# Performance work log

Measured on AMD Instinct MI355X. Metric: run time of the kernel, lower is better.

Reference implementation:

```python
import jax, jax.numpy as jnp
import numpy as np

NODE_DIM, HIDDEN_DIM, OUT_DIM = 64, 128, 64
N_NODES, N_EDGES = 50000, 800000
SLOPE = 0.05


def leaky(x):
    return jnp.where(x >= 0, x, SLOPE * x)


def setup_inputs() -> dict:
    key = jax.random.key(0)
    ks = jax.random.split(key, 8)
    x = jax.random.normal(ks[0], (N_NODES, NODE_DIM), dtype=jnp.float32)
    edge_index = jax.random.randint(ks[1], (2, N_EDGES), 0, N_NODES, dtype=jnp.int64)
    s0 = 1.0 / np.sqrt(NODE_DIM)
    s1 = 1.0 / np.sqrt(HIDDEN_DIM)
    W0 = jax.random.uniform(ks[2], (NODE_DIM, HIDDEN_DIM), jnp.float32, -s0, s0)
    b0 = jax.random.uniform(ks[3], (HIDDEN_DIM,), jnp.float32, -s0, s0)
    W1 = jax.random.uniform(ks[4], (HIDDEN_DIM, HIDDEN_DIM), jnp.float32, -s1, s1)
    b1 = jax.random.uniform(ks[5], (HIDDEN_DIM,), jnp.float32, -s1, s1)
    W2 = jax.random.uniform(ks[6], (HIDDEN_DIM, OUT_DIM), jnp.float32, -s1, s1)
    b2 = jax.random.uniform(ks[7], (OUT_DIM,), jnp.float32, -s1, s1)
    return {"x": x, "edge_index": edge_index, "W0": W0, "b0": b0,
            "W1": W1, "b1": b1, "W2": W2, "b2": b2}


def reference(x, edge_index, W0, b0, W1, b1, W2, b2):
    # gather-sum: [E, node_dim]
    e = x[edge_index[0]] + x[edge_index[1]]
    h = leaky(e @ W0 + b0)          # [E, hidden]
    h = leaky(h @ W1 + b1)          # [E, hidden]
    out = leaky(h @ W2 + b2)        # [E, out]
    return out
```

## Files before the change

### kernel.cpp

```cpp
#include <hip/hip_runtime.h>

typedef _Float16 half8  __attribute__((ext_vector_type(8)));
typedef float    floatx4 __attribute__((ext_vector_type(4)));

#define N_NODES 50000
#define N_EDGES 800000
#define SLOPE 0.05f

#define WS_Z   0ull
#define WS_W1  (WS_Z  + (size_t)N_NODES * 128 * 2)
#define WS_W2  (WS_W1 + 128 * 128 * 2)
#define WS_B0  (WS_W2 + 64 * 128 * 2)
#define WS_B1  (WS_B0 + 128 * 4)
#define WS_B2  (WS_B1 + 128 * 4)

#define W0_STRIDE 72
#define H_STRIDE 136
#define HC_STRIDE 40

__device__ __forceinline__ float leaky(float t) { return t >= 0.f ? t : SLOPE * t; }

__global__ void wprep_kernel(const float* __restrict__ W1, const float* __restrict__ W2,
                             const float* __restrict__ b0, const float* __restrict__ b1,
                             const float* __restrict__ b2, unsigned char* __restrict__ ws) {
    _Float16* wt1 = (_Float16*)(ws + WS_W1);
    _Float16* wt2 = (_Float16*)(ws + WS_W2);
    float* B0 = (float*)(ws + WS_B0);
    float* B1 = (float*)(ws + WS_B1);
    float* B2 = (float*)(ws + WS_B2);
    int t = blockIdx.x * 1024 + threadIdx.x;
    if (t < 16384) {
        int k = t >> 7, n = t & 127;
        wt1[n * 128 + k] = (_Float16)W1[k * 128 + n];
    } else if (t < 24576) {
        int i = t - 16384;
        int k = i >> 6, n = i & 63;
        wt2[n * 128 + k] = (_Float16)W2[k * 64 + n];
    } else if (t < 24576 + 320) {
        int i = t - 24576;
        if (i < 128) B0[i] = b0[i];
        else if (i < 256) B1[i - 128] = b1[i - 128];
        else B2[i - 256] = b2[i - 256];
    }
}

__global__ __launch_bounds__(512, 4) void z_kernel(const float* __restrict__ x,
                                                   const float* __restrict__ W0,
                                                   unsigned char* __restrict__ ws) {
    __shared__ __align__(16) _Float16 w0t[128 * W0_STRIDE];
    __shared__ __align__(16) _Float16 hbuf[8][16 * H_STRIDE];
    _Float16* __restrict__ z = (_Float16*)(ws + WS_Z);

    {
        int t = threadIdx.x;
        int n = t >> 2, k0 = (t & 3) * 16;
        half8 t0, t1;
        #pragma unroll
        for (int j = 0; j < 8; ++j) t0[j] = (_Float16)W0[(k0 + j) * 128 + n];
        #pragma unroll
        for (int j = 0; j < 8; ++j) t1[j] = (_Float16)W0[(k0 + 8 + j) * 128 + n];
        *(half8*)&w0t[n * W0_STRIDE + k0] = t0;
        *(half8*)&w0t[n * W0_STRIDE + k0 + 8] = t1;
    }
    __syncthreads();

    const int wave = threadIdx.x >> 6, lane = threadIdx.x & 63;
    const int cl = lane & 15, q = lane >> 4;
    const int rowbase = blockIdx.x * 128 + wave * 16;
    int row = rowbase + cl; if (row > N_NODES - 1) row = N_NODES - 1;

    half8 a[2];
    #pragma unroll
    for (int ks = 0; ks < 2; ++ks) {
        const floatx4* px = (const floatx4*)(x + (size_t)row * 64 + ks * 32 + q * 8);
        floatx4 u0 = px[0], u1 = px[1];
        #pragma unroll
        for (int j = 0; j < 4; ++j) { a[ks][j] = (_Float16)u0[j]; a[ks][4 + j] = (_Float16)u1[j]; }
    }

    _Float16* hs = &hbuf[wave][0];
    #pragma unroll
    for (int n = 0; n < 8; ++n) {
        floatx4 c = {0.f, 0.f, 0.f, 0.f};
        #pragma unroll
        for (int ks = 0; ks < 2; ++ks) {
            half8 b = *(const half8*)&w0t[(n * 16 + cl) * W0_STRIDE + ks * 32 + q * 8];
            c = __builtin_amdgcn_mfma_f32_16x16x32_f16(a[ks], b, c, 0, 0, 0);
        }
        #pragma unroll
        for (int r = 0; r < 4; ++r)
            hs[(q * 4 + r) * H_STRIDE + n * 16 + cl] = (_Float16)c[r];
    }

    int rl = lane >> 2, ch = lane & 3;
    int grow = rowbase + rl;
    if (grow < N_NODES) {
        #pragma unroll
        for (int i = 0; i < 4; ++i)
            *(half8*)(z + (size_t)grow * 128 + i * 32 + ch * 8) =
                *(const half8*)&hs[rl * H_STRIDE + i * 32 + ch * 8];
    }
}

__global__ __launch_bounds__(512, 4) void edge_kernel(const int* __restrict__ ei,
                                                      const unsigned char* __restrict__ ws,
                                                      float* __restrict__ out) {
    __shared__ __align__(16) _Float16 w1s[128 * H_STRIDE];
    __shared__ __align__(16) _Float16 w2s[64 * H_STRIDE];
    __shared__ __align__(16) _Float16 hc[8][16 * HC_STRIDE];
    __shared__ float b0s[128], b1s[128], b2s[64];

    const _Float16* __restrict__ z    = (const _Float16*)(ws + WS_Z);
    const _Float16* __restrict__ wt1g = (const _Float16*)(ws + WS_W1);
    const _Float16* __restrict__ wt2g = (const _Float16*)(ws + WS_W2);

    {
        int t = threadIdx.x;
        #pragma unroll
        for (int it = 0; it < 4; ++it) {
            int c = t + it * 512;
            int row = c >> 4, cc = c & 15;
            *(half8*)&w1s[row * H_STRIDE + cc * 8] = *(const half8*)&wt1g[row * 128 + cc * 8];
        }
        #pragma unroll
        for (int it = 0; it < 2; ++it) {
            int c = t + it * 512;
            int row = c >> 4, cc = c & 15;
            *(half8*)&w2s[row * H_STRIDE + cc * 8] = *(const half8*)&wt2g[row * 128 + cc * 8];
        }
        if (t < 128) {
            b0s[t] = *(const float*)(ws + WS_B0 + t * 4);
            b1s[t] = *(const float*)(ws + WS_B1 + t * 4);
        } else if (t < 192) {
            b2s[t - 128] = *(const float*)(ws + WS_B2 + (size_t)(t - 128) * 4);
        }
    }
    __syncthreads();

    const int wave = threadIdx.x >> 6, lane = threadIdx.x & 63;
    const int cl = lane & 15, q = lane >> 4;
    const int rowbase = blockIdx.x * 128 + wave * 16;

    const int r = rowbase + cl;
    const int s = ei[r];
    const int d = ei[N_EDGES + r];
    const _Float16* zs = z + (size_t)s * 128;
    const _Float16* zd = z + (size_t)d * 128;

    half8 a1[4];
    #pragma unroll
    for (int ks = 0; ks < 4; ++ks) {
        half8 u = *(const half8*)(zs + ks * 32 + q * 8);
        half8 v = *(const half8*)(zd + ks * 32 + q * 8);
        floatx4 bA = *(const floatx4*)&b0s[ks * 32 + q * 8];
        floatx4 bB = *(const floatx4*)&b0s[ks * 32 + q * 8 + 4];
        #pragma unroll
        for (int j = 0; j < 4; ++j) {
            float t0 = (float)u[j]     + (float)v[j]     + bA[j];
            float t1 = (float)u[4 + j] + (float)v[4 + j] + bB[j];
            a1[ks][j]     = (_Float16)leaky(t0);
            a1[ks][4 + j] = (_Float16)leaky(t1);
        }
    }

    _Float16* hw = &hc[wave][0];
    floatx4 acc2[4];
    #pragma unroll
    for (int n2 = 0; n2 < 4; ++n2) acc2[n2] = (floatx4){0.f, 0.f, 0.f, 0.f};

    #pragma unroll
    for (int ks = 0; ks < 4; ++ks) {
        #pragma unroll
        for (int nn = 0; nn < 2; ++nn) {
            const int n = ks * 2 + nn;
            floatx4 c = {0.f, 0.f, 0.f, 0.f};
            #pragma unroll
            for (int kk = 0; kk < 4; ++kk) {
                half8 b = *(const half8*)&w1s[(n * 16 + cl) * H_STRIDE + kk * 32 + q * 8];
                c = __builtin_amdgcn_mfma_f32_16x16x32_f16(a1[kk], b, c, 0, 0, 0);
            }
            const float bb = b1s[n * 16 + cl];
            #pragma unroll
            for (int rr = 0; rr < 4; ++rr)
                hw[(q * 4 + rr) * HC_STRIDE + nn * 16 + cl] = (_Float16)leaky(c[rr] + bb);
        }
        half8 a2 = *(const half8*)&hw[cl * HC_STRIDE + q * 8];
        #pragma unroll
        for (int n2 = 0; n2 < 4; ++n2) {
            half8 b = *(const half8*)&w2s[(n2 * 16 + cl) * H_STRIDE + ks * 32 + q * 8];
            acc2[n2] = __builtin_amdgcn_mfma_f32_16x16x32_f16(a2, b, acc2[n2], 0, 0, 0);
        }
    }

    #pragma unroll
    for (int n2 = 0; n2 < 4; ++n2) {
        const float bb = b2s[n2 * 16 + cl];
        #pragma unroll
        for (int rr = 0; rr < 4; ++rr)
            out[(size_t)(rowbase + q * 4 + rr) * 64 + n2 * 16 + cl] = leaky(acc2[n2][rr] + bb);
    }
}

extern "C" void kernel_launch(void* const* d_in, const int* in_sizes, int n_in,
                              void* d_out, int out_size, void* d_ws, size_t ws_size,
                              hipStream_t stream) {
    const float* x  = (const float*)d_in[0];
    const int*   ei = (const int*)d_in[1];
    const float* W0 = (const float*)d_in[2];
    const float* b0 = (const float*)d_in[3];
    const float* W1 = (const float*)d_in[4];
    const float* b1 = (const float*)d_in[5];
    const float* W2 = (const float*)d_in[6];
    const float* b2 = (const float*)d_in[7];
    float* out = (float*)d_out;
    unsigned char* ws = (unsigned char*)d_ws;

    wprep_kernel<<<25, 1024, 0, stream>>>(W1, W2, b0, b1, b2, ws);
    z_kernel<<<(N_NODES + 127) / 128, 512, 0, stream>>>(x, W0, ws);
    edge_kernel<<<N_EDGES / 128, 512, 0, stream>>>(ei, ws, out);
}
```

Baseline: 295.3 us.

## Make edge kernel persistent with two M-tiles per wave and index prefetch

```diff
diff --git a/kernel.cpp b/kernel.cpp
--- a/kernel.cpp
+++ b/kernel.cpp
@@ -6,6 +6,8 @@
 #define N_NODES 50000
 #define N_EDGES 800000
 #define SLOPE 0.05f
+#define GRID 512
+#define NT 3125
 
 #define WS_Z   0ull
 #define WS_W1  (WS_Z  + (size_t)N_NODES * 128 * 2)
@@ -13,6 +15,7 @@
 #define WS_B0  (WS_W2 + 64 * 128 * 2)
 #define WS_B1  (WS_B0 + 128 * 4)
 #define WS_B2  (WS_B1 + 128 * 4)
+#define WS_W0T (WS_B2 + 64 * 4)
 
 #define W0_STRIDE 72
 #define H_STRIDE 136
@@ -20,11 +23,13 @@
 
 __device__ __forceinline__ float leaky(float t) { return t >= 0.f ? t : SLOPE * t; }
 
-__global__ void wprep_kernel(const float* __restrict__ W1, const float* __restrict__ W2,
-                             const float* __restrict__ b0, const float* __restrict__ b1,
-                             const float* __restrict__ b2, unsigned char* __restrict__ ws) {
+__global__ void wprep_kernel(const float* __restrict__ W0, const float* __restrict__ W1,
+                             const float* __restrict__ W2, const float* __restrict__ b0,
+                             const float* __restrict__ b1, const float* __restrict__ b2,
+                             unsigned char* __restrict__ ws) {
     _Float16* wt1 = (_Float16*)(ws + WS_W1);
     _Float16* wt2 = (_Float16*)(ws + WS_W2);
+    _Float16* w0t = (_Float16*)(ws + WS_W0T);
     float* B0 = (float*)(ws + WS_B0);
     float* B1 = (float*)(ws + WS_B1);
     float* B2 = (float*)(ws + WS_B2);
@@ -36,8 +41,12 @@
         int i = t - 16384;
         int k = i >> 6, n = i & 63;
         wt2[n * 128 + k] = (_Float16)W2[k * 64 + n];
-    } else if (t < 24576 + 320) {
+    } else if (t < 32768) {
         int i = t - 24576;
+        int n = i >> 6, k = i & 63;
+        w0t[n * 64 + k] = (_Float16)W0[k * 128 + n];
+    } else if (t < 32768 + 320) {
+        int i = t - 32768;
         if (i < 128) B0[i] = b0[i];
         else if (i < 256) B1[i - 128] = b1[i - 128];
         else B2[i - 256] = b2[i - 256];
@@ -45,22 +54,20 @@
 }
 
 __global__ __launch_bounds__(512, 4) void z_kernel(const float* __restrict__ x,
-                                                   const float* __restrict__ W0,
                                                    unsigned char* __restrict__ ws) {
-    __shared__ __align__(16) _Float16 w0t[128 * W0_STRIDE];
+    __shared__ __align__(16) _Float16 w0s[128 * W0_STRIDE];
     __shared__ __align__(16) _Float16 hbuf[8][16 * H_STRIDE];
     _Float16* __restrict__ z = (_Float16*)(ws + WS_Z);
+    const _Float16* __restrict__ w0t = (const _Float16*)(ws + WS_W0T);
 
     {
         int t = threadIdx.x;
-        int n = t >> 2, k0 = (t & 3) * 16;
-        half8 t0, t1;
-        #pragma unroll
-        for (int j = 0; j < 8; ++j) t0[j] = (_Float16)W0[(k0 + j) * 128 + n];
-        #pragma unroll
-        for (int j = 0; j < 8; ++j) t1[j] = (_Float16)W0[(k0 + 8 + j) * 128 + n];
-        *(half8*)&w0t[n * W0_STRIDE + k0] = t0;
-        *(half8*)&w0t[n * W0_STRIDE + k0 + 8] = t1;
+        #pragma unroll
+        for (int it = 0; it < 2; ++it) {
+            int c = t + it * 512;
+            int row = c >> 3, cc = c & 7;
+            *(half8*)&w0s[row * W0_STRIDE + cc * 8] = *(const half8*)&w0t[row * 64 + cc * 8];
+        }
     }
     __syncthreads();
 
@@ -84,7 +91,7 @@
         floatx4 c = {0.f, 0.f, 0.f, 0.f};
         #pragma unroll
         for (int ks = 0; ks < 2; ++ks) {
-            half8 b = *(const half8*)&w0t[(n * 16 + cl) * W0_STRIDE + ks * 32 + q * 8];
+            half8 b = *(const half8*)&w0s[(n * 16 + cl) * W0_STRIDE + ks * 32 + q * 8];
             c = __builtin_amdgcn_mfma_f32_16x16x32_f16(a[ks], b, c, 0, 0, 0);
         }
         #pragma unroll
@@ -139,65 +146,107 @@
 
     const int wave = threadIdx.x >> 6, lane = threadIdx.x & 63;
     const int cl = lane & 15, q = lane >> 4;
-    const int rowbase = blockIdx.x * 128 + wave * 16;
-
-    const int r = rowbase + cl;
-    const int s = ei[r];
-    const int d = ei[N_EDGES + r];
-    const _Float16* zs = z + (size_t)s * 128;
-    const _Float16* zd = z + (size_t)d * 128;
-
-    half8 a1[4];
-    #pragma unroll
-    for (int ks = 0; ks < 4; ++ks) {
-        half8 u = *(const half8*)(zs + ks * 32 + q * 8);
-        half8 v = *(const half8*)(zd + ks * 32 + q * 8);
-        floatx4 bA = *(const floatx4*)&b0s[ks * 32 + q * 8];
-        floatx4 bB = *(const floatx4*)&b0s[ks * 32 + q * 8 + 4];
-        #pragma unroll
-        for (int j = 0; j < 4; ++j) {
-            float t0 = (float)u[j]     + (float)v[j]     + bA[j];
-            float t1 = (float)u[4 + j] + (float)v[4 + j] + bB[j];
-            a1[ks][j]     = (_Float16)leaky(t0);
-            a1[ks][4 + j] = (_Float16)leaky(t1);
-        }
-    }
-
     _Float16* hw = &hc[wave][0];
-    floatx4 acc2[4];
-    #pragma unroll
-    for (int n2 = 0; n2 < 4; ++n2) acc2[n2] = (floatx4){0.f, 0.f, 0.f, 0.f};
-
-    #pragma unroll
-    for (int ks = 0; ks < 4; ++ks) {
-        #pragma unroll
-        for (int nn = 0; nn < 2; ++nn) {
-            const int n = ks * 2 + nn;
-            floatx4 c = {0.f, 0.f, 0.f, 0.f};
-            #pragma unroll
-            for (int kk = 0; kk < 4; ++kk) {
-                half8 b = *(const half8*)&w1s[(n * 16 + cl) * H_STRIDE + kk * 32 + q * 8];
-                c = __builtin_amdgcn_mfma_f32_16x16x32_f16(a1[kk], b, c, 0, 0, 0);
-            }
-            const float bb = b1s[n * 16 + cl];
-            #pragma unroll
-            for (int rr = 0; rr < 4; ++rr)
-                hw[(q * 4 + rr) * HC_STRIDE + nn * 16 + cl] = (_Float16)leaky(c[rr] + bb);
-        }
-        half8 a2 = *(const half8*)&hw[cl * HC_STRIDE + q * 8];
+
+    int tile = blockIdx.x;
+    int s0, d0, s1, d1;
+    {
+        int r = tile * 256 + wave * 32 + cl;
+        s0 = ei[r];           d0 = ei[N_EDGES + r];
+        s1 = ei[r + 16];      d1 = ei[N_EDGES + r + 16];
+    }
+
+    while (tile < NT) {
+        const int next = tile + GRID;
+        int ns0 = s0, nd0 = d0, ns1 = s1, nd1 = d1;
+        if (next < NT) {
+            int r = next * 256 + wave * 32 + cl;
+            ns0 = ei[r];      nd0 = ei[N_EDGES + r];
+            ns1 = ei[r + 16]; nd1 = ei[N_EDGES + r + 16];
+        }
+
+        const int eb = tile * 256 + wave * 32;
+
+        const _Float16* zs0 = z + (size_t)s0 * 128;
+        const _Float16* zd0 = z + (size_t)d0 * 128;
+        const _Float16* zs1 = z + (size_t)s1 * 128;
+        const _Float16* zd1 = z + (size_t)d1 * 128;
+
+        half8 a1lo[4], a1hi[4];
+        #pragma unroll
+        for (int ks = 0; ks < 4; ++ks) {
+            half8 u = *(const half8*)(zs0 + ks * 32 + q * 8);
+            half8 v = *(const half8*)(zd0 + ks * 32 + q * 8);
+            half8 u2 = *(const half8*)(zs1 + ks * 32 + q * 8);
+            half8 v2 = *(const half8*)(zd1 + ks * 32 + q * 8);
+            floatx4 bA = *(const floatx4*)&b0s[ks * 32 + q * 8];
+            floatx4 bB = *(const floatx4*)&b0s[ks * 32 + q * 8 + 4];
+            #pragma unroll
+            for (int j = 0; j < 4; ++j) {
+                a1lo[ks][j]     = (_Float16)leaky((float)u[j]      + (float)v[j]      + bA[j]);
+                a1lo[ks][4 + j] = (_Float16)leaky((float)u[4 + j]  + (float)v[4 + j]  + bB[j]);
+                a1hi[ks][j]     = (_Float16)leaky((float)u2[j]     + (float)v2[j]     + bA[j]);
+                a1hi[ks][4 + j] = (_Float16)leaky((float)u2[4 + j] + (float)v2[4 + j] + bB[j]);
+            }
+        }
+
+        floatx4 acc2lo[4], acc2hi[4];
         #pragma unroll
         for (int n2 = 0; n2 < 4; ++n2) {
-            half8 b = *(const half8*)&w2s[(n2 * 16 + cl) * H_STRIDE + ks * 32 + q * 8];
-            acc2[n2] = __builtin_amdgcn_mfma_f32_16x16x32_f16(a2, b, acc2[n2], 0, 0, 0);
-        }
-    }
-
-    #pragma unroll
-    for (int n2 = 0; n2 < 4; ++n2) {
-        const float bb = b2s[n2 * 16 + cl];
-        #pragma unroll
-        for (int rr = 0; rr < 4; ++rr)
-            out[(size_t)(rowbase + q * 4 + rr) * 64 + n2 * 16 + cl] = leaky(acc2[n2][rr] + bb);
+            acc2lo[n2] = (floatx4){0.f, 0.f, 0.f, 0.f};
+            acc2hi[n2] = (floatx4){0.f, 0.f, 0.f, 0.f};
+        }
+
+        #pragma unroll
+        for (int ks = 0; ks < 4; ++ks) {
+            floatx4 kc[2];
+            #pragma unroll
+            for (int nn = 0; nn < 2; ++nn) {
+                const int n = ks * 2 + nn;
+                floatx4 c0 = {0.f, 0.f, 0.f, 0.f};
+                floatx4 c1 = {0.f, 0.f, 0.f, 0.f};
+                #pragma unroll
+                for (int kk = 0; kk < 4; ++kk) {
+                    half8 b = *(const half8*)&w1s[(n * 16 + cl) * H_STRIDE + kk * 32 + q * 8];
+                    c0 = __builtin_amdgcn_mfma_f32_16x16x32_f16(a1lo[kk], b, c0, 0, 0, 0);
+                    c1 = __builtin_amdgcn_mfma_f32_16x16x32_f16(a1hi[kk], b, c1, 0, 0, 0);
+                }
+                const float bb = b1s[n * 16 + cl];
+                #pragma unroll
+                for (int rr = 0; rr < 4; ++rr)
+                    hw[(q * 4 + rr) * HC_STRIDE + nn * 16 + cl] = (_Float16)leaky(c0[rr] + bb);
+                kc[nn] = c1;
+            }
+            half8 a2lo = *(const half8*)&hw[cl * HC_STRIDE + q * 8];
+            #pragma unroll
+            for (int nn = 0; nn < 2; ++nn) {
+                const float bb = b1s[(ks * 2 + nn) * 16 + cl];
+                #pragma unroll
+                for (int rr = 0; rr < 4; ++rr)
+                    hw[(q * 4 + rr) * HC_STRIDE + nn * 16 + cl] = (_Float16)leaky(kc[nn][rr] + bb);
+            }
+            half8 a2hi = *(const half8*)&hw[cl * HC_STRIDE + q * 8];
+
+            #pragma unroll
+            for (int n2 = 0; n2 < 4; ++n2) {
+                half8 b = *(const half8*)&w2s[(n2 * 16 + cl) * H_STRIDE + ks * 32 + q * 8];
+                acc2lo[n2] = __builtin_amdgcn_mfma_f32_16x16x32_f16(a2lo, b, acc2lo[n2], 0, 0, 0);
+                acc2hi[n2] = __builtin_amdgcn_mfma_f32_16x16x32_f16(a2hi, b, acc2hi[n2], 0, 0, 0);
+            }
+        }
+
+        #pragma unroll
+        for (int n2 = 0; n2 < 4; ++n2) {
+            const float bb = b2s[n2 * 16 + cl];
+            #pragma unroll
+            for (int rr = 0; rr < 4; ++rr) {
+                out[(size_t)(eb + q * 4 + rr) * 64 + n2 * 16 + cl]      = leaky(acc2lo[n2][rr] + bb);
+                out[(size_t)(eb + 16 + q * 4 + rr) * 64 + n2 * 16 + cl] = leaky(acc2hi[n2][rr] + bb);
+            }
+        }
+
+        tile = next;
+        s0 = ns0; d0 = nd0; s1 = ns1; d1 = nd1;
     }
 }
 
@@ -215,7 +264,7 @@
     float* out = (float*)d_out;
     unsigned char* ws = (unsigned char*)d_ws;
 
-    wprep_kernel<<<25, 1024, 0, stream>>>(W1, W2, b0, b1, b2, ws);
-    z_kernel<<<(N_NODES + 127) / 128, 512, 0, stream>>>(x, W0, ws);
-    edge_kernel<<<N_EDGES / 128, 512, 0, stream>>>(ei, ws, out);
-}
+    wprep_kernel<<<33, 1024, 0, stream>>>(W0, W1, W2, b0, b1, b2, ws);
+    z_kernel<<<(N_NODES + 127) / 128, 512, 0, stream>>>(x, ws);
+    edge_kernel<<<GRID, 512, 0, stream>>>(ei, ws, out);
+}
```

Measured after the change: 345.9 us. 17.1% more time.
